# Performance work log

Measured on AMD Instinct MI355X. Metric: run time of the kernel, lower is better.

The kernel has to match this reference:

```python
import jax, jax.numpy as jnp
import numpy as np

DIM = 1024
HEADS = 16
HEAD_DIM = DIM // HEADS
B, T = 4, 2048
BASE = 10000.0
EPS = 1e-5


def rotate_half(x):
    x1, x2 = x[..., : x.shape[-1] // 2], x[..., x.shape[-1] // 2 :]
    return jnp.concatenate((-x2, x1), axis=-1)


def setup_inputs() -> dict:
    key = jax.random.key(0)
    ks = jax.random.split(key, 7)
    x = jax.random.normal(ks[0], (B, T, DIM), dtype=jnp.float32)
    attention_mask = jnp.ones((B, T), dtype=jnp.int32)
    s = 1.0 / np.sqrt(DIM)
    Wq = jax.random.normal(ks[1], (DIM, DIM), dtype=jnp.float32) * s
    Wk = jax.random.normal(ks[2], (DIM, DIM), dtype=jnp.float32) * s
    Wv = jax.random.normal(ks[3], (DIM, DIM), dtype=jnp.float32) * s
    Wo = jax.random.normal(ks[4], (DIM, DIM), dtype=jnp.float32) * s
    gamma = jnp.ones((DIM,), dtype=jnp.float32)
    beta = jnp.zeros((DIM,), dtype=jnp.float32)
    return {"x": x, "attention_mask": attention_mask, "Wq": Wq, "Wk": Wk,
            "Wv": Wv, "Wo": Wo, "gamma": gamma, "beta": beta}


def reference(x, attention_mask, Wq, Wk, Wv, Wo, gamma, beta):
    Bsz, Tlen, D = x.shape
    H, HD = HEADS, HEAD_DIM
    scale = HD ** -0.5

    # projections (nn.Linear: y = x @ W.T)
    def proj(W):
        y = jnp.einsum("btd,ed->bte", x, W)
        return y.reshape(Bsz, Tlen, H, HD).transpose(0, 2, 1, 3)  # b h t hd

    q, k, v = proj(Wq), proj(Wk), proj(Wv)

    # RoPE cos/sin cache
    inv_freq = 1.0 / (BASE ** (jnp.arange(0, HD, 2, dtype=jnp.float32) / HD))
    t = jnp.arange(Tlen, dtype=jnp.float32)
    freqs = jnp.einsum("i,j->ij", t, inv_freq)        # (T, HD/2)
    emb = jnp.concatenate((freqs, freqs), axis=-1)    # (T, HD)
    cos = jnp.cos(emb)[None, None]                    # (1,1,T,HD)
    sin = jnp.sin(emb)[None, None]

    q = q * cos + rotate_half(q) * sin
    k = k * cos + rotate_half(k) * sin

    attn = jnp.einsum("bhqd,bhkd->bhqk", q, k) * scale
    additive = (1.0 - attention_mask.astype(jnp.float32))[:, None, None, :]
    attn = attn - additive * 1e9
    attn = jax.nn.softmax(attn, axis=-1)
    out = jnp.einsum("bhqk,bhkd->bhqd", attn, v)
    out = out.transpose(0, 2, 1, 3).reshape(Bsz, Tlen, D)
    out = jnp.einsum("btd,ed->bte", out, Wo)

    # residual + LayerNorm
    h = x + out
    mu = jnp.mean(h, axis=-1, keepdims=True)
    var = jnp.mean((h - mu) ** 2, axis=-1, keepdims=True)
    return (h - mu) * jax.lax.rsqrt(var + EPS) * gamma + beta
```

## Files before the change

### kernel.cpp

```cpp
#include <hip/hip_runtime.h>
#include <hip/hip_bf16.h>
#include <math.h>

#define DIM    1024
#define HEADS  16
#define HD     64
#define BSZ    4
#define SEQ    2048
#define NTOK   (BSZ*SEQ)

typedef __attribute__((ext_vector_type(4))) float f32x4;
typedef __attribute__((ext_vector_type(8))) short bf16x8;

__device__ __forceinline__ unsigned short f2bf(float f){
  union { float f; unsigned int i; } v; v.f = f;
  unsigned int u = v.i;
  u += 0x7fffu + ((u >> 16) & 1u);
  return (unsigned short)(u >> 16);
}
__device__ __forceinline__ void gld_lds16(const void* g, void* l){
  __builtin_amdgcn_global_load_lds(
      (const __attribute__((address_space(1))) unsigned int*)g,
      (__attribute__((address_space(3))) unsigned int*)l, 16, 0, 0);
}

__global__ __launch_bounds__(256) void cvt_bf16(const float* __restrict__ src,
                                                unsigned short* __restrict__ dst, int n4){
  int i = blockIdx.x*256 + threadIdx.x;
  if (i < n4){
    float4 v = ((const float4*)src)[i];
    ushort4 o;
    o.x = f2bf(v.x); o.y = f2bf(v.y); o.z = f2bf(v.z); o.w = f2bf(v.w);
    ((ushort4*)dst)[i] = o;
  }
}

__global__ __launch_bounds__(256) void cvt_w4(
    const float* __restrict__ wq, const float* __restrict__ wk,
    const float* __restrict__ wv, const float* __restrict__ wo,
    unsigned short* __restrict__ dst){
  int i = blockIdx.x*256 + threadIdx.x;
  int which = i >> 18;
  int j = i & ((1<<18)-1);
  const float* src = which==0 ? wq : which==1 ? wk : which==2 ? wv : wo;
  float4 v = ((const float4*)src)[j];
  ushort4 o;
  o.x = f2bf(v.x); o.y = f2bf(v.y); o.z = f2bf(v.z); o.w = f2bf(v.w);
  ((ushort4*)dst)[i] = o;
}

__global__ __launch_bounds__(256) void rope_tab(float* __restrict__ ctab,
                                                float* __restrict__ stab){
  int i = blockIdx.x*256 + threadIdx.x;
  int t = i >> 5, j = i & 31;
  float freq = (float)t * powf(10000.0f, -(float)j * (1.0f/32.0f));
  ctab[i] = cosf(freq);
  stab[i] = sinf(freq);
}

template<int MODE>
__global__ __launch_bounds__(256) void gemm_bt(
    const unsigned short* __restrict__ A,
    const unsigned short* __restrict__ Bw,
    const float* __restrict__ ctab, const float* __restrict__ stab,
    const float* __restrict__ xres,
    unsigned short* __restrict__ outb,
    float* __restrict__ outf,
    int M, int N, int K)
{
  __shared__ unsigned short As[128*64];
  __shared__ unsigned short Bs[128*64];
  const int tid = threadIdx.x;
  const int w = tid >> 6, l = tid & 63;
  const int lr = l & 15, lg = l >> 4;
  const int nbm = M >> 7;
  const int bm = blockIdx.x % nbm;
  const int bn = blockIdx.x / nbm;
  const int wr = w >> 1, wc = w & 1;
  const int srow = l >> 3;
  const int scol = (l & 7) * 8;

  const f32x4 fzero = {0.f,0.f,0.f,0.f};
  f32x4 acc[4][4];
#pragma unroll
  for (int mt = 0; mt < 4; ++mt)
#pragma unroll
    for (int nt = 0; nt < 4; ++nt) acc[mt][nt] = fzero;

  const size_t abase = (size_t)(bm*128)*K;
  const size_t bbase = (size_t)(bn*128)*K;

  for (int k0 = 0; k0 < K; k0 += 64) {
    __syncthreads();
#pragma unroll
    for (int ci = 0; ci < 4; ++ci) {
      int c = w*4 + ci;
      int row = c*8 + srow;
      gld_lds16(A  + abase + (size_t)row*K + k0 + scol, (char*)As + c*1024);
      gld_lds16(Bw + bbase + (size_t)row*K + k0 + scol, (char*)Bs + c*1024);
    }
    __syncthreads();
#pragma unroll
    for (int ks = 0; ks < 2; ++ks) {
      bf16x8 af[4], bfr[4];
#pragma unroll
      for (int mt = 0; mt < 4; ++mt)
        af[mt] = *(const bf16x8*)(As + (wr*64 + mt*16 + lr)*64 + ks*32 + lg*8);
#pragma unroll
      for (int nt = 0; nt < 4; ++nt)
        bfr[nt] = *(const bf16x8*)(Bs + (wc*64 + nt*16 + lr)*64 + ks*32 + lg*8);
#pragma unroll
      for (int mt = 0; mt < 4; ++mt)
#pragma unroll
        for (int nt = 0; nt < 4; ++nt)
          acc[mt][nt] = __builtin_amdgcn_mfma_f32_16x16x32_bf16(af[mt], bfr[nt], acc[mt][nt], 0, 0, 0);
    }
  }

  const int mb = bm*128 + wr*64;
  const int nb = bn*128 + wc*64;
  if (MODE == 0) {
    const int which = nb >> 10;
    const int h = (nb & 1023) >> 6;
    const size_t secbase = (size_t)which * ((size_t)BSZ*HEADS*SEQ*HD);
#pragma unroll
    for (int mt = 0; mt < 4; ++mt) {
#pragma unroll
      for (int r = 0; r < 4; ++r) {
        int m = mb + mt*16 + lg*4 + r;
        int b = m >> 11, t = m & (SEQ-1);
        float v[4];
#pragma unroll
        for (int nt = 0; nt < 4; ++nt) v[nt] = acc[mt][nt][r];
        if (which < 2) {
#pragma unroll
          for (int nt = 0; nt < 2; ++nt) {
            int hd = nt*16 + lr;
            float c = ctab[t*32 + hd], s = stab[t*32 + hd];
            float v0 = v[nt], v1 = v[nt+2];
            v[nt]   = v0*c - v1*s;
            v[nt+2] = v1*c + v0*s;
          }
          if (which == 0) {
#pragma unroll
            for (int nt = 0; nt < 4; ++nt) v[nt] *= 0.125f;
          }
        }
        size_t ob = secbase + ((size_t)(b*HEADS + h)*SEQ + t) * HD;
#pragma unroll
        for (int nt = 0; nt < 4; ++nt)
          outb[ob + nt*16 + lr] = f2bf(v[nt]);
      }
    }
  } else {
#pragma unroll
    for (int mt = 0; mt < 4; ++mt) {
#pragma unroll
      for (int r = 0; r < 4; ++r) {
        int m = mb + mt*16 + lg*4 + r;
        size_t rowb = (size_t)m * DIM;
#pragma unroll
        for (int nt = 0; nt < 4; ++nt) {
          int n = nb + nt*16 + lr;
          outf[rowb + n] = acc[mt][nt][r] + xres[rowb + n];
        }
      }
    }
  }
}

__global__ __launch_bounds__(256) void vtrans(
    const unsigned short* __restrict__ vin,
    unsigned short* __restrict__ vT)
{
  __shared__ unsigned short T[64][65];
  const int tid = threadIdx.x;
  const int bh = blockIdx.x >> 5;
  const int t0 = (blockIdx.x & 31) * 64;
  const unsigned short* src = vin + ((size_t)bh*SEQ + t0) * HD;
  for (int i = tid; i < 512; i += 256) {
    int r = i >> 3, c8 = (i & 7) * 8;
    *(bf16x8*)(&T[r][c8]) = *(const bf16x8*)(src + r*HD + c8);
  }
  __syncthreads();
  for (int i = tid; i < 512; i += 256) {
    int d = i >> 3, tc8 = (i & 7) * 8;
    bf16x8 o;
#pragma unroll
    for (int j = 0; j < 8; ++j) ((unsigned short*)&o)[j] = T[tc8+j][d];
    *(bf16x8*)(vT + ((size_t)bh*HD + d)*SEQ + t0 + tc8) = o;
  }
}

__global__ __launch_bounds__(256) void attn_fwd(
    const unsigned short* __restrict__ qkv,
    const unsigned short* __restrict__ vT,
    const int* __restrict__ amask,
    unsigned short* __restrict__ aout)
{
  __shared__ unsigned short Kls[64*64];
  __shared__ unsigned short Vls[64*64];
  __shared__ unsigned short Pls[64*72];
  const int tid = threadIdx.x;
  const int w = tid >> 6, l = tid & 63;
  const int lr = l & 15, lg = l >> 4;
  const int bh = blockIdx.x >> 5;
  const int qb = blockIdx.x & 31;
  const int b = bh >> 4;
  const size_t SEC = (size_t)BSZ*HEADS*SEQ*HD;
  const unsigned short* Qp = qkv + (size_t)bh*SEQ*HD;
  const unsigned short* Kp = Qp + SEC;
  const unsigned short* Vp = vT + (size_t)bh*HD*SEQ;

  const int srow   = l >> 3;
  const int schunk = ((l & 7) ^ srow) * 8;

  const int qrow = qb*64 + w*16 + lr;
  bf16x8 qf[2];
#pragma unroll
  for (int ks = 0; ks < 2; ++ks)
    qf[ks] = *(const bf16x8*)(Qp + (size_t)qrow*HD + ks*32 + lg*8);

  const f32x4 fzero = {0.f,0.f,0.f,0.f};
  f32x4 o[4];
#pragma unroll
  for (int dt = 0; dt < 4; ++dt) o[dt] = fzero;
  float mrun[4], lrun[4];
#pragma unroll
  for (int r = 0; r < 4; ++r){ mrun[r] = -1e30f; lrun[r] = 0.f; }

  for (int kt = 0; kt < SEQ/64; ++kt) {
    __syncthreads();
#pragma unroll
    for (int c = 0; c < 2; ++c) {
      const int rb = (c*4 + w)*8;
      gld_lds16(Kp + (size_t)(kt*64 + rb + srow)*HD + schunk,
                (char*)Kls + (c*4 + w)*1024);
      gld_lds16(Vp + (size_t)(rb + srow)*SEQ + kt*64 + schunk,
                (char*)Vls + (c*4 + w)*1024);
    }
    __syncthreads();

    f32x4 s[4];
#pragma unroll
    for (int nt = 0; nt < 4; ++nt) s[nt] = fzero;
#pragma unroll
    for (int ks = 0; ks < 2; ++ks) {
#pragma unroll
      for (int nt = 0; nt < 4; ++nt) {
        bf16x8 kf = *(const bf16x8*)(&Kls[(nt*16+lr)*64 + (((ks*4+lg) ^ (lr&7))*8)]);
        s[nt] = __builtin_amdgcn_mfma_f32_16x16x32_bf16(qf[ks], kf, s[nt], 0, 0, 0);
      }
    }

    float addm[4];
#pragma unroll
    for (int nt = 0; nt < 4; ++nt)
      addm[nt] = (1.0f - (float)amask[b*SEQ + kt*64 + nt*16 + lr]) * 1e9f;
    float corr[4];
    float pv[4][4];
#pragma unroll
    for (int r = 0; r < 4; ++r) {
      float mx = -1e30f;
#pragma unroll
      for (int nt = 0; nt < 4; ++nt) {
        float vv = s[nt][r] - addm[nt];
        pv[nt][r] = vv;
        mx = fmaxf(mx, vv);
      }
#pragma unroll
      for (int d = 8; d >= 1; d >>= 1) mx = fmaxf(mx, __shfl_xor(mx, d));
      float mnew = fmaxf(mrun[r], mx);
      corr[r] = __expf(mrun[r] - mnew);
      float rsum = 0.f;
#pragma unroll
      for (int nt = 0; nt < 4; ++nt) {
        float p = __expf(pv[nt][r] - mnew);
        pv[nt][r] = p;
        rsum += p;
      }
#pragma unroll
      for (int d = 8; d >= 1; d >>= 1) rsum += __shfl_xor(rsum, d);
      lrun[r] = lrun[r] * corr[r] + rsum;
      mrun[r] = mnew;
    }
#pragma unroll
    for (int dt = 0; dt < 4; ++dt)
#pragma unroll
      for (int r = 0; r < 4; ++r)
        o[dt][r] *= corr[r];

#pragma unroll
    for (int nt = 0; nt < 4; ++nt)
#pragma unroll
      for (int r = 0; r < 4; ++r)
        Pls[(w*16 + lg*4 + r)*72 + nt*16 + lr] = f2bf(pv[nt][r]);

#pragma unroll
    for (int ks = 0; ks < 2; ++ks) {
      bf16x8 pf = *(const bf16x8*)(&Pls[(w*16+lr)*72 + ks*32 + lg*8]);
#pragma unroll
      for (int dt = 0; dt < 4; ++dt) {
        bf16x8 vf = *(const bf16x8*)(&Vls[(dt*16+lr)*64 + (((ks*4+lg) ^ (lr&7))*8)]);
        o[dt] = __builtin_amdgcn_mfma_f32_16x16x32_bf16(pf, vf, o[dt], 0, 0, 0);
      }
    }
  }

  const int h = bh & (HEADS-1);
#pragma unroll
  for (int r = 0; r < 4; ++r) {
    float inv = 1.0f / lrun[r];
    int t = qb*64 + w*16 + lg*4 + r;
    size_t rowb = (size_t)(b*SEQ + t) * DIM + h*HD;
#pragma unroll
    for (int dt = 0; dt < 4; ++dt)
      aout[rowb + dt*16 + lr] = f2bf(o[dt][r] * inv);
  }
}

__global__ __launch_bounds__(256) void layernorm_inplace(
    float* __restrict__ hbuf,
    const float* __restrict__ gamma, const float* __restrict__ beta)
{
  const int row = blockIdx.x;
  const int tid = threadIdx.x;
  const int w = tid >> 6, l = tid & 63;
  __shared__ float red[8];
  float* hr = hbuf + (size_t)row * DIM;
  float4 v = *(const float4*)(hr + tid*4);
  float s = v.x+v.y+v.z+v.w;
#pragma unroll
  for (int d = 32; d >= 1; d >>= 1) s += __shfl_xor(s, d);
  if (l == 0) red[w] = s;
  __syncthreads();
  float mu = (red[0]+red[1]+red[2]+red[3]) * (1.0f/DIM);
  float d0=v.x-mu, d1=v.y-mu, d2=v.z-mu, d3=v.w-mu;
  float q = d0*d0+d1*d1+d2*d2+d3*d3;
#pragma unroll
  for (int d = 32; d >= 1; d >>= 1) q += __shfl_xor(q, d);
  if (l == 0) red[4+w] = q;
  __syncthreads();
  float var = (red[4]+red[5]+red[6]+red[7]) * (1.0f/DIM);
  float rstd = rsqrtf(var + 1e-5f);
  int c = tid*4;
  float4 ou;
  ou.x = d0*rstd*gamma[c+0]+beta[c+0];
  ou.y = d1*rstd*gamma[c+1]+beta[c+1];
  ou.z = d2*rstd*gamma[c+2]+beta[c+2];
  ou.w = d3*rstd*gamma[c+3]+beta[c+3];
  *(float4*)(hr + c) = ou;
}

extern "C" void kernel_launch(void* const* d_in, const int* in_sizes, int n_in,
                              void* d_out, int out_size, void* d_ws, size_t ws_size,
                              hipStream_t stream) {
  const float* x     = (const float*)d_in[0];
  const int*   amask = (const int*)  d_in[1];
  const float* Wq    = (const float*)d_in[2];
  const float* Wk    = (const float*)d_in[3];
  const float* Wv    = (const float*)d_in[4];
  const float* Wo    = (const float*)d_in[5];
  const float* gamma = (const float*)d_in[6];
  const float* beta  = (const float*)d_in[7];

  unsigned short* xb   = (unsigned short*)d_ws;
  unsigned short* Wqkv = xb + (size_t)NTOK*DIM;
  unsigned short* Wob  = Wqkv + (size_t)3*DIM*DIM;
  unsigned short* qkv  = Wob + (size_t)DIM*DIM;
  unsigned short* aout = qkv + (size_t)3*NTOK*DIM;
  float* ctab = (float*)(aout + (size_t)NTOK*DIM);
  float* stab = ctab + SEQ*32;

  unsigned short* vT = xb;
  float* hout = (float*)d_out;

  cvt_bf16<<<(NTOK*DIM/4 + 255)/256, 256, 0, stream>>>(x, xb, NTOK*DIM/4);
  cvt_w4<<<4*DIM*DIM/4/256, 256, 0, stream>>>(Wq, Wk, Wv, Wo, Wqkv);
  rope_tab<<<SEQ*32/256, 256, 0, stream>>>(ctab, stab);

  gemm_bt<0><<<(NTOK/128)*(3*DIM/128), 256, 0, stream>>>(
      xb, Wqkv, ctab, stab, nullptr, qkv, nullptr, NTOK, 3*DIM, DIM);

  vtrans<<<BSZ*HEADS*(SEQ/64), 256, 0, stream>>>(qkv + (size_t)2*BSZ*HEADS*SEQ*HD, vT);

  attn_fwd<<<BSZ*HEADS*(SEQ/64), 256, 0, stream>>>(qkv, vT, amask, aout);

  gemm_bt<1><<<(NTOK/128)*(DIM/128), 256, 0, stream>>>(
      aout, Wob, nullptr, nullptr, x, nullptr, hout, NTOK, DIM, DIM);

  layernorm_inplace<<<NTOK, 256, 0, stream>>>(hout, gamma, beta);
}
```

Before: 456.1 us.

## Use lazy softmax max rescaling and precompute additive mask in attention

Adds a kernel that precomputes the additive float mask once instead of converting the int mask in every attention tile. The online softmax now skips the cross-lane max reduction and the rescaling of the output accumulator unless some row's new max exceeds the running max by more than a threshold, checked with a wave-wide vote. The row-sum reduction is deferred to the epilogue, and probabilities are truncated to bf16 so the sum matches what goes into the MFMA. This cuts shuffles and exps per tile but adds a branch, and the exp arguments can reach up to the threshold above zero, which slightly loosens numeric headroom.

Measured after the change: 376.1 us. 1.21x faster.

```diff
diff --git a/kernel.cpp b/kernel.cpp
--- a/kernel.cpp
+++ b/kernel.cpp
@@ -56,6 +56,12 @@
   float freq = (float)t * powf(10000.0f, -(float)j * (1.0f/32.0f));
   ctab[i] = cosf(freq);
   stab[i] = sinf(freq);
+}
+
+__global__ __launch_bounds__(256) void cvt_mask(const int* __restrict__ am,
+                                                float* __restrict__ out, int n){
+  int i = blockIdx.x*256 + threadIdx.x;
+  if (i < n) out[i] = (1.0f - (float)am[i]) * 1e9f;
 }
 
 template<int MODE>
@@ -195,7 +201,7 @@
 __global__ __launch_bounds__(256) void attn_fwd(
     const unsigned short* __restrict__ qkv,
     const unsigned short* __restrict__ vT,
-    const int* __restrict__ amask,
+    const float* __restrict__ maskadd,
     unsigned short* __restrict__ aout)
 {
   __shared__ unsigned short Kls[64*64];
@@ -253,48 +259,49 @@
       }
     }
 
-    float addm[4];
-#pragma unroll
-    for (int nt = 0; nt < 4; ++nt)
-      addm[nt] = (1.0f - (float)amask[b*SEQ + kt*64 + nt*16 + lr]) * 1e9f;
-    float corr[4];
     float pv[4][4];
 #pragma unroll
+    for (int nt = 0; nt < 4; ++nt) {
+      float am = maskadd[b*SEQ + kt*64 + nt*16 + lr];
+#pragma unroll
+      for (int r = 0; r < 4; ++r)
+        pv[nt][r] = s[nt][r] - am;
+    }
+
+    float excess = 0.f;
+#pragma unroll
     for (int r = 0; r < 4; ++r) {
-      float mx = -1e30f;
+      float mx = fmaxf(fmaxf(pv[0][r], pv[1][r]), fmaxf(pv[2][r], pv[3][r]));
+      excess = fmaxf(excess, mx - mrun[r]);
+    }
+    if (!__all(excess <= 8.0f)) {
+#pragma unroll
+      for (int r = 0; r < 4; ++r) {
+        float rm = fmaxf(fmaxf(pv[0][r], pv[1][r]), fmaxf(pv[2][r], pv[3][r]));
+#pragma unroll
+        for (int d = 8; d >= 1; d >>= 1) rm = fmaxf(rm, __shfl_xor(rm, d));
+        float mnew = fmaxf(mrun[r], rm);
+        float corr = __expf(mrun[r] - mnew);
+        lrun[r] *= corr;
+        mrun[r] = mnew;
+#pragma unroll
+        for (int dt = 0; dt < 4; ++dt) o[dt][r] *= corr;
+      }
+    }
+
+#pragma unroll
+    for (int r = 0; r < 4; ++r) {
+      float sum = 0.f;
 #pragma unroll
       for (int nt = 0; nt < 4; ++nt) {
-        float vv = s[nt][r] - addm[nt];
-        pv[nt][r] = vv;
-        mx = fmaxf(mx, vv);
-      }
-#pragma unroll
-      for (int d = 8; d >= 1; d >>= 1) mx = fmaxf(mx, __shfl_xor(mx, d));
-      float mnew = fmaxf(mrun[r], mx);
-      corr[r] = __expf(mrun[r] - mnew);
-      float rsum = 0.f;
-#pragma unroll
-      for (int nt = 0; nt < 4; ++nt) {
-        float p = __expf(pv[nt][r] - mnew);
-        pv[nt][r] = p;
-        rsum += p;
-      }
-#pragma unroll
-      for (int d = 8; d >= 1; d >>= 1) rsum += __shfl_xor(rsum, d);
-      lrun[r] = lrun[r] * corr[r] + rsum;
-      mrun[r] = mnew;
-    }
-#pragma unroll
-    for (int dt = 0; dt < 4; ++dt)
-#pragma unroll
-      for (int r = 0; r < 4; ++r)
-        o[dt][r] *= corr[r];
-
-#pragma unroll
-    for (int nt = 0; nt < 4; ++nt)
-#pragma unroll
-      for (int r = 0; r < 4; ++r)
-        Pls[(w*16 + lg*4 + r)*72 + nt*16 + lr] = f2bf(pv[nt][r]);
+        float p = __expf(pv[nt][r] - mrun[r]);
+        union { float f; unsigned int u; } cv; cv.f = p;
+        cv.u &= 0xffff0000u;
+        sum += cv.f;
+        Pls[(w*16 + lg*4 + r)*72 + nt*16 + lr] = (unsigned short)(cv.u >> 16);
+      }
+      lrun[r] += sum;
+    }
 
 #pragma unroll
     for (int ks = 0; ks < 2; ++ks) {
@@ -310,7 +317,10 @@
   const int h = bh & (HEADS-1);
 #pragma unroll
   for (int r = 0; r < 4; ++r) {
-    float inv = 1.0f / lrun[r];
+    float lsum = lrun[r];
+#pragma unroll
+    for (int d = 8; d >= 1; d >>= 1) lsum += __shfl_xor(lsum, d);
+    float inv = 1.0f / lsum;
     int t = qb*64 + w*16 + lg*4 + r;
     size_t rowb = (size_t)(b*SEQ + t) * DIM + h*HD;
 #pragma unroll
@@ -371,6 +381,7 @@
   unsigned short* aout = qkv + (size_t)3*NTOK*DIM;
   float* ctab = (float*)(aout + (size_t)NTOK*DIM);
   float* stab = ctab + SEQ*32;
+  float* madd = stab + SEQ*32;
 
   unsigned short* vT = xb;
   float* hout = (float*)d_out;
@@ -378,13 +389,14 @@
   cvt_bf16<<<(NTOK*DIM/4 + 255)/256, 256, 0, stream>>>(x, xb, NTOK*DIM/4);
   cvt_w4<<<4*DIM*DIM/4/256, 256, 0, stream>>>(Wq, Wk, Wv, Wo, Wqkv);
   rope_tab<<<SEQ*32/256, 256, 0, stream>>>(ctab, stab);
+  cvt_mask<<<(NTOK + 255)/256, 256, 0, stream>>>(amask, madd, NTOK);
 
   gemm_bt<0><<<(NTOK/128)*(3*DIM/128), 256, 0, stream>>>(
       xb, Wqkv, ctab, stab, nullptr, qkv, nullptr, NTOK, 3*DIM, DIM);
 
   vtrans<<<BSZ*HEADS*(SEQ/64), 256, 0, stream>>>(qkv + (size_t)2*BSZ*HEADS*SEQ*HD, vT);
 
-  attn_fwd<<<BSZ*HEADS*(SEQ/64), 256, 0, stream>>>(qkv, vT, amask, aout);
+  attn_fwd<<<BSZ*HEADS*(SEQ/64), 256, 0, stream>>>(qkv, vT, madd, aout);
 
   gemm_bt<1><<<(NTOK/128)*(DIM/128), 256, 0, stream>>>(
       aout, Wob, nullptr, nullptr, x, nullptr, hout, NTOK, DIM, DIM);
```
